# Kernel optimization log

Measured on AMD Instinct MI355X. Metric: run time of the kernel, lower is better.

## Reference

```python
import jax, jax.numpy as jnp
import numpy as np

N, E, F, H = 20000, 320000, 128, 256   # nodes, edges, in-features, hidden
M, NQ = 4096, 2048                      # lsq rows, QP variables
LAMB_MAX = 2.0


def setup_inputs() -> dict:
    key = jax.random.key(0)
    ks = jax.random.split(key, 12)
    x = jax.random.normal(ks[0], (N, F), jnp.float32)
    edge_index = jax.random.randint(ks[1], (2, E), 0, N)
    A = jax.random.normal(ks[2], (M, NQ), jnp.float32) * 0.05
    b = jax.random.normal(ks[3], (M, 1), jnp.float32)
    feat_ids = jax.random.randint(ks[4], (NQ,), 0, N)
    x_prior = jax.random.uniform(ks[5], (NQ, 1), jnp.float32)
    lamb = jnp.ones((1,), jnp.float32)
    # ChebConv K=2 weights: one linear per Chebyshev order, plus bias
    W10 = jax.random.normal(ks[6], (F, H), jnp.float32) / np.sqrt(F)
    W11 = jax.random.normal(ks[7], (F, H), jnp.float32) / np.sqrt(F)
    b1 = jnp.zeros((H,), jnp.float32)
    W20 = jax.random.normal(ks[8], (H, 1), jnp.float32) / np.sqrt(H)
    W21 = jax.random.normal(ks[9], (H, 1), jnp.float32) / np.sqrt(H)
    b2 = jnp.zeros((1,), jnp.float32)
    return {"x": x, "edge_index": edge_index, "A": A, "b": b,
            "feat_ids": feat_ids, "x_prior": x_prior, "lamb": lamb,
            "W10": W10, "W11": W11, "b1": b1,
            "W20": W20, "W21": W21, "b2": b2}


def _cheb_conv(x, edge_index, W0, W1, bias, lam_max):
    """PyG ChebConv with K=2: out = x @ W0 + (2L/lam_max - I) x @ W1 + bias,
    L = I - D^{-1/2} A D^{-1/2}, via edge gather/scatter (no dense NxN)."""
    row, col = edge_index[0], edge_index[1]
    n = x.shape[0]
    deg = jax.ops.segment_sum(jnp.ones_like(row, dtype=x.dtype), row, num_segments=n)
    dinv = jnp.where(deg > 0, deg ** -0.5, 0.0)
    # normalized edge weight scaled by 2/lam_max, negated (off-diag of L_hat)
    w = -(2.0 / lam_max) * dinv[row] * dinv[col]              # [E]
    msg = jax.ops.segment_sum(w[:, None] * x[col], row, num_segments=n)
    Tx1 = msg + (2.0 / lam_max - 1.0) * x                      # diagonal of L_hat
    return x @ W0 + Tx1 @ W1 + bias


def reference(x, edge_index, A, b, feat_ids, x_prior, lamb,
              W10, W11, b1, W20, W21, b2):
    h = jax.nn.relu(_cheb_conv(x, edge_index, W10, W11, b1, LAMB_MAX))
    h = lamb[0] * jax.nn.relu(_cheb_conv(h, edge_index, W20, W21, b2, LAMB_MAX))
    hfold = h[feat_ids] + 1e-5                                 # [NQ, 1]
    q = hfold[:, 0]
    # QP: min 1/2 z^T Q z + p^T z with vacuous inequality (0*z <= 0.1) and no
    # equality constraints -> interior-point converges to unconstrained min.
    Q = A.T @ A + jnp.diag(q)                                  # [NQ, NQ]
    p = -(x_prior * hfold)[:, 0] - (b.T @ A)[0]                # [NQ]
    z = jnp.linalg.solve(Q, -p)                                # [NQ]
    return z[:, None]                                          # f.T -> [NQ, 1]
```

## Files before the change

kernel.cpp:

```cpp
#include <hip/hip_runtime.h>

#define N_NODES 20000
#define N_EDGES 320000
#define F_DIM   128
#define H_DIM   256
#define M_ROWS  4096
#define NQ      2048
#define NIT     18
#define MM_ROWS 20032

typedef __attribute__((ext_vector_type(8))) short short8;
typedef __attribute__((ext_vector_type(4))) float f32x4;


__device__ __forceinline__ float wred(float v) {
#pragma unroll
  for (int m = 32; m > 0; m >>= 1) v += __shfl_xor(v, m, 64);
  return v;
}

__device__ __forceinline__ float bred256(float v, float* lds) {
  v = wred(v);
  int w = threadIdx.x >> 6;
  if ((threadIdx.x & 63) == 0) lds[w] = v;
  __syncthreads();
  float tot = lds[0] + lds[1] + lds[2] + lds[3];
  __syncthreads();
  return tot;
}

__device__ __forceinline__ unsigned f2bf(float f) {
  unsigned u = __float_as_uint(f);
  unsigned r = u + 0x7fffu + ((u >> 16) & 1u);
  return r >> 16;
}
__device__ __forceinline__ float bflo(unsigned u) { return __uint_as_float(u << 16); }
__device__ __forceinline__ float bfhi(unsigned u) { return __uint_as_float(u & 0xffff0000u); }


__global__ __launch_bounds__(256) void k_deg(const int* __restrict__ ei, int* __restrict__ deg) {
  int e = blockIdx.x * 256 + threadIdx.x;
  if (e < N_EDGES) atomicAdd(&deg[ei[e]], 1);
}

__global__ __launch_bounds__(1024) void k_scan(const int* __restrict__ deg,
    int* __restrict__ rowstart, float* __restrict__ dinv) {
  __shared__ int part[1024];
  int t = threadIdx.x;
  const int chunk = (N_NODES + 1023) / 1024;
  int lo = t * chunk;
  int hi = lo + chunk; if (hi > N_NODES) hi = N_NODES;
  int s = 0;
  for (int i = lo; i < hi; ++i) {
    int d = deg[i];
    dinv[i] = d > 0 ? rsqrtf((float)d) : 0.f;
    s += d;
  }
  part[t] = s;
  __syncthreads();
  for (int off = 1; off < 1024; off <<= 1) {
    int v = part[t];
    int add = (t >= off) ? part[t - off] : 0;
    __syncthreads();
    part[t] = v + add;
    __syncthreads();
  }
  int base = (t > 0) ? part[t - 1] : 0;
  for (int i = lo; i < hi; ++i) { rowstart[i] = base; base += deg[i]; }
  if (t == 0) rowstart[N_NODES] = part[1023];
}

__global__ __launch_bounds__(256) void k_scatter(const int* __restrict__ ei,
    const int* __restrict__ rowstart, int* __restrict__ cursor,
    const float* __restrict__ dinv, int* __restrict__ cols, float* __restrict__ wvals) {
  int e = blockIdx.x * 256 + threadIdx.x;
  if (e >= N_EDGES) return;
  int r = ei[e];
  int c = ei[N_EDGES + e];
  int pos = rowstart[r] + atomicAdd(&cursor[r], 1);
  cols[pos] = c;
  wvals[pos] = -dinv[r] * dinv[c];
}

#define CONVX_BLKS (MM_ROWS * 16 / 256)

__global__ __launch_bounds__(256) void k_pack(const float* __restrict__ x,
    const float* __restrict__ W10, const float* __restrict__ W11,
    unsigned* __restrict__ xu, unsigned* __restrict__ Wtb) {
  int bx = blockIdx.x;
  if (bx < CONVX_BLKS) {
    int gid = bx * 256 + threadIdx.x;
    int row = gid >> 4;
    int q8 = gid & 15;
    uint4* xu4 = (uint4*)xu;
    if (row < N_NODES) {
      const float4* x4 = (const float4*)x;
      float4 a = x4[(size_t)row * 32 + q8 * 2];
      float4 b = x4[(size_t)row * 32 + q8 * 2 + 1];
      uint4 u;
      u.x = f2bf(a.x) | (f2bf(a.y) << 16);
      u.y = f2bf(a.z) | (f2bf(a.w) << 16);
      u.z = f2bf(b.x) | (f2bf(b.y) << 16);
      u.w = f2bf(b.z) | (f2bf(b.w) << 16);
      xu4[(size_t)row * 32 + q8] = u;
    } else {
      uint4 z = make_uint4(0, 0, 0, 0);
      xu4[(size_t)row * 32 + q8] = z;
      xu4[(size_t)row * 32 + 16 + q8] = z;
    }
  } else {
    int gid = (bx - CONVX_BLKS) * 256 + threadIdx.x;
    int n = gid >> 7;
    int u = gid & 127;
    int k0 = u * 2;
    float v0 = (k0 < 128) ? W10[(size_t)k0 * H_DIM + n]
                          : W11[(size_t)(k0 - 128) * H_DIM + n];
    float v1 = (k0 + 1 < 128) ? W10[(size_t)(k0 + 1) * H_DIM + n]
                              : W11[(size_t)(k0 - 127) * H_DIM + n];
    Wtb[(size_t)n * 128 + u] = f2bf(v0) | (f2bf(v1) << 16);
  }
}

__global__ __launch_bounds__(256) void k_msg1(const int* __restrict__ rowstart,
    const int* __restrict__ cols, const float* __restrict__ wvals,
    unsigned* __restrict__ xu) {
  int wid = (blockIdx.x * 256 + threadIdx.x) >> 6;
  int lane = threadIdx.x & 63;
  if (wid >= N_NODES) return;
  int s0 = rowstart[wid], s1 = rowstart[wid + 1];
  float2 acc = make_float2(0.f, 0.f);
  for (int e = s0; e < s1; ++e) {
    int c = cols[e];
    float w = wvals[e];
    unsigned u = xu[(size_t)c * 128 + lane];
    acc.x += w * bflo(u);
    acc.y += w * bfhi(u);
  }
  xu[(size_t)wid * 128 + 64 + lane] = f2bf(acc.x) | (f2bf(acc.y) << 16);
}

#define WS_ST 20

__global__ __launch_bounds__(256) void k_mm(const unsigned* __restrict__ xu,
    const unsigned* __restrict__ Wtb, const float* __restrict__ b1,
    const float* __restrict__ W20, const float* __restrict__ W21,
    float* __restrict__ t, float* __restrict__ s) {
  __shared__ unsigned Ws[2][256 * WS_ST];
  const int row0 = blockIdx.x * 64;
  const int tid = threadIdx.x;
  const int w = tid >> 6, lane = tid & 63;
  const int colb = w * 64;
  const int frow = lane & 15, fqo = (lane >> 4) * 4;
  const int c16 = lane & 15, q4 = lane >> 4;

  f32x4 acc[4][4];
#pragma unroll
  for (int a = 0; a < 4; ++a)
#pragma unroll
    for (int b = 0; b < 4; ++b) {
      acc[a][b][0] = 0.f; acc[a][b][1] = 0.f;
      acc[a][b][2] = 0.f; acc[a][b][3] = 0.f;
    }

  const uint4* Wtb4 = (const uint4*)Wtb;
  uint4 rw[4];
#pragma unroll
  for (int j = 0; j < 4; ++j) rw[j] = Wtb4[(size_t)tid * 32 + j];

  for (int kc = 0; kc < 8; ++kc) {
    const int b = kc & 1;
    unsigned* dst = Ws[b] + tid * WS_ST;
#pragma unroll
    for (int j = 0; j < 4; ++j) *(uint4*)(dst + j * 4) = rw[j];
    if (kc + 1 < 8) {
#pragma unroll
      for (int j = 0; j < 4; ++j) rw[j] = Wtb4[(size_t)tid * 32 + (kc + 1) * 4 + j];
    }
    __syncthreads();
    short8 af[4], bf[4];
#pragma unroll
    for (int a = 0; a < 4; ++a)
      af[a] = *(const short8*)(xu + (size_t)(row0 + a * 16 + frow) * 128 + kc * 16 + fqo);
#pragma unroll
    for (int n = 0; n < 4; ++n)
      bf[n] = *(const short8*)(Ws[b] + (colb + n * 16 + frow) * WS_ST + fqo);
#pragma unroll
    for (int a = 0; a < 4; ++a)
#pragma unroll
      for (int n = 0; n < 4; ++n)
        acc[a][n] = __builtin_amdgcn_mfma_f32_16x16x32_bf16(af[a], bf[n], acc[a][n], 0, 0, 0);
    __syncthreads();
  }

  float tp[4][4] = {}, sp[4][4] = {};
#pragma unroll
  for (int b2 = 0; b2 < 4; ++b2) {
    int gc = colb + b2 * 16 + c16;
    float w20 = W20[gc], w21 = W21[gc], bb = b1[gc];
#pragma unroll
    for (int a = 0; a < 4; ++a)
#pragma unroll
      for (int r = 0; r < 4; ++r) {
        float val = acc[a][b2][r] + bb;
        val = val > 0.f ? val : 0.f;
        tp[a][r] += val * w20;
        sp[a][r] += val * w21;
      }
  }
#pragma unroll
  for (int a = 0; a < 4; ++a)
#pragma unroll
    for (int r = 0; r < 4; ++r) {
#pragma unroll
      for (int m = 1; m < 16; m <<= 1) {
        tp[a][r] += __shfl_xor(tp[a][r], m, 64);
        sp[a][r] += __shfl_xor(sp[a][r], m, 64);
      }
    }
  if (c16 == 0) {
#pragma unroll
    for (int a = 0; a < 4; ++a)
#pragma unroll
      for (int r = 0; r < 4; ++r) {
        int gr = row0 + a * 16 + q4 * 4 + r;
        if (gr < N_NODES) {
          atomicAdd(&t[gr], tp[a][r]);
          atomicAdd(&s[gr], sp[a][r]);
        }
      }
  }
}


__global__ __launch_bounds__(256) void k_h2(const float* __restrict__ t,
    const float* __restrict__ s, const int* __restrict__ rowstart,
    const int* __restrict__ cols, const float* __restrict__ wvals,
    const float* __restrict__ lamb, const float* __restrict__ b2, float* __restrict__ h2) {
  int i = blockIdx.x * 256 + threadIdx.x;
  if (i >= N_NODES) return;
  float m = 0.f;
  int s0 = rowstart[i], s1 = rowstart[i + 1];
  for (int e = s0; e < s1; ++e) m += wvals[e] * s[cols[e]];
  float val = t[i] + m + b2[0];
  val = val > 0.f ? val : 0.f;
  h2[i] = lamb[0] * val;
}

__global__ __launch_bounds__(256) void k_prep(const float* __restrict__ A,
    const float* __restrict__ b, unsigned* __restrict__ Atu, float* __restrict__ btA_parts) {
  int jp = blockIdx.x * 256 + threadIdx.x;
  int k0 = blockIdx.y * 128;
  const float2* A2 = (const float2*)A;
  float acc0 = 0.f, acc1 = 0.f;
  for (int kk = 0; kk < 128; kk += 8) {
    float ax[8], ay[8];
#pragma unroll
    for (int i = 0; i < 8; ++i) {
      int k = k0 + kk + i;
      float2 a = A2[(size_t)k * 1024 + jp];
      float bk = b[k];
      acc0 += a.x * bk;
      acc1 += a.y * bk;
      ax[i] = a.x; ay[i] = a.y;
    }
    uint4 t0, t1;
    t0.x = f2bf(ax[0]) | (f2bf(ax[1]) << 16);
    t0.y = f2bf(ax[2]) | (f2bf(ax[3]) << 16);
    t0.z = f2bf(ax[4]) | (f2bf(ax[5]) << 16);
    t0.w = f2bf(ax[6]) | (f2bf(ax[7]) << 16);
    t1.x = f2bf(ay[0]) | (f2bf(ay[1]) << 16);
    t1.y = f2bf(ay[2]) | (f2bf(ay[3]) << 16);
    t1.z = f2bf(ay[4]) | (f2bf(ay[5]) << 16);
    t1.w = f2bf(ay[6]) | (f2bf(ay[7]) << 16);
    int uoff = (k0 + kk) >> 1;
    *(uint4*)(Atu + (size_t)(2 * jp) * 2048 + uoff) = t0;
    *(uint4*)(Atu + (size_t)(2 * jp + 1) * 2048 + uoff) = t1;
  }
  ((float2*)(btA_parts + (size_t)blockIdx.y * NQ))[jp] = make_float2(acc0, acc1);
}

__global__ __launch_bounds__(256) void k_qrhs(const float* __restrict__ h2,
    const int* __restrict__ feat_ids, const float* __restrict__ x_prior,
    const float* __restrict__ btA_parts, float* __restrict__ q, float* __restrict__ r) {
  int j = blockIdx.x * 256 + threadIdx.x;
  int f = feat_ids[j];
  float hf = h2[f] + 1e-5f;
  q[j] = hf;
  float bta = 0.f;
#pragma unroll
  for (int c = 0; c < 32; ++c) bta += btA_parts[(size_t)c * NQ + j];
  r[j] = x_prior[j] * hf + bta;
}

#define GR_ST 20

__global__ __launch_bounds__(512) void k_gram(const unsigned* __restrict__ Atu,
                                              float* __restrict__ Gp) {
  __shared__ unsigned shmem[10240];
  const int i0 = blockIdx.x * 128, j0 = blockIdx.y * 128;
  const int kz = blockIdx.z;
  const int tid = threadIdx.x;
  const int grp = tid >> 8;
  const int t8 = tid & 255;
  const int w = tid >> 6;
  const int wt = w & 3;
  const int lane = tid & 63;
  const int wr = (wt >> 1) * 64, wc = (wt & 1) * 64;
  const int srow = t8 >> 1, suo = (t8 & 1) * 8;
  const int frow = lane & 15, fqo = (lane >> 4) * 4;

  unsigned* shA = shmem + grp * 5120;
  unsigned* shB = shA + 2560;

  f32x4 acc[4][4];
#pragma unroll
  for (int a = 0; a < 4; ++a)
#pragma unroll
    for (int b = 0; b < 4; ++b) {
      acc[a][b][0] = 0.f; acc[a][b][1] = 0.f;
      acc[a][b][2] = 0.f; acc[a][b][3] = 0.f;
    }

  const unsigned* pa = Atu + (size_t)(i0 + srow) * 2048 + kz * 1024 + suo;
  const unsigned* pb = Atu + (size_t)(j0 + srow) * 2048 + kz * 1024 + suo;

  int ku = grp * 16;
  uint4 ra0 = *(const uint4*)(pa + ku);
  uint4 ra1 = *(const uint4*)(pa + ku + 4);
  uint4 rb0 = *(const uint4*)(pb + ku);
  uint4 rb1 = *(const uint4*)(pb + ku + 4);

  for (int si = 0; si < 32; ++si) {
    unsigned* as = shA + srow * GR_ST + suo;
    unsigned* bs = shB + srow * GR_ST + suo;
    *(uint4*)as = ra0; *(uint4*)(as + 4) = ra1;
    *(uint4*)bs = rb0; *(uint4*)(bs + 4) = rb1;
    if (si + 1 < 32) {
      ku = (si + 1) * 32 + grp * 16;
      ra0 = *(const uint4*)(pa + ku);
      ra1 = *(const uint4*)(pa + ku + 4);
      rb0 = *(const uint4*)(pb + ku);
      rb1 = *(const uint4*)(pb + ku + 4);
    }
    __syncthreads();
    short8 af[4], bf[4];
#pragma unroll
    for (int a = 0; a < 4; ++a)
      af[a] = *(const short8*)(shA + (wr + a * 16 + frow) * GR_ST + fqo);
#pragma unroll
    for (int b2 = 0; b2 < 4; ++b2)
      bf[b2] = *(const short8*)(shB + (wc + b2 * 16 + frow) * GR_ST + fqo);
#pragma unroll
    for (int a = 0; a < 4; ++a)
#pragma unroll
      for (int b2 = 0; b2 < 4; ++b2)
        acc[a][b2] = __builtin_amdgcn_mfma_f32_16x16x32_bf16(af[a], bf[b2], acc[a][b2], 0, 0, 0);
    __syncthreads();
  }

  const int q4 = lane >> 4, c16 = lane & 15;
  float* comb = (float*)shmem;
#pragma unroll
  for (int rnd = 0; rnd < 2; ++rnd) {
    if (grp == 1 && (wt >> 1) == rnd) {
      float* dst = comb + (wt & 1) * 4160;
#pragma unroll
      for (int a = 0; a < 4; ++a)
#pragma unroll
        for (int b2 = 0; b2 < 4; ++b2)
#pragma unroll
          for (int r = 0; r < 4; ++r)
            dst[(a * 16 + q4 * 4 + r) * 65 + b2 * 16 + c16] = acc[a][b2][r];
    }
    __syncthreads();
    if (grp == 0 && (wt >> 1) == rnd) {
      const float* src = comb + (wt & 1) * 4160;
#pragma unroll
      for (int a = 0; a < 4; ++a)
#pragma unroll
        for (int b2 = 0; b2 < 4; ++b2)
#pragma unroll
          for (int r = 0; r < 4; ++r)
            acc[a][b2][r] += src[(a * 16 + q4 * 4 + r) * 65 + b2 * 16 + c16];
    }
    __syncthreads();
  }

  if (grp == 0) {
    float* Gz = Gp + (size_t)kz * NQ * NQ;
#pragma unroll
    for (int a = 0; a < 4; ++a)
#pragma unroll
      for (int b2 = 0; b2 < 4; ++b2)
#pragma unroll
        for (int r = 0; r < 4; ++r) {
          int gr = i0 + wr + a * 16 + q4 * 4 + r;
          int gc = j0 + wc + b2 * 16 + c16;
          Gz[(size_t)gr * NQ + gc] = acc[a][b2][r];
        }
  }
}

__global__ __launch_bounds__(256) void k_gconv(const float* __restrict__ G0,
    const float* __restrict__ G1, const float* __restrict__ q,
    unsigned* __restrict__ Gb, float* __restrict__ qcorr) {
  int row = blockIdx.x;
  int tid = threadIdx.x;
  const float4* g04 = (const float4*)(G0 + (size_t)row * NQ);
  const float4* g14 = (const float4*)(G1 + (size_t)row * NQ);
  float4 a0 = g04[tid * 2], b0 = g04[tid * 2 + 1];
  float4 a1 = g14[tid * 2], b1 = g14[tid * 2 + 1];
  float v[8] = {a0.x + a1.x, a0.y + a1.y, a0.z + a1.z, a0.w + a1.w,
                b0.x + b1.x, b0.y + b1.y, b0.z + b1.z, b0.w + b1.w};
  bool diag = ((row >> 3) == tid);
  if (diag) v[row & 7] += q[row];
  uint4 u;
  u.x = f2bf(v[0]) | (f2bf(v[1]) << 16);
  u.y = f2bf(v[2]) | (f2bf(v[3]) << 16);
  u.z = f2bf(v[4]) | (f2bf(v[5]) << 16);
  u.w = f2bf(v[6]) | (f2bf(v[7]) << 16);
  ((uint4*)(Gb + (size_t)row * 1024))[tid] = u;
  if (diag) {
    float vd = v[row & 7];
    qcorr[row] = vd - __uint_as_float(f2bf(vd) << 16);
  }
}

__global__ __launch_bounds__(256) void k_cgG(int k, const unsigned* __restrict__ Gb,
    const float* __restrict__ qcorr,
    const float* __restrict__ r_old, float* __restrict__ r_new,
    const float* __restrict__ p_old, float* __restrict__ p_new,
    const float* __restrict__ Qp_in, float* __restrict__ Qp_out,
    float* __restrict__ xcg) {
  __shared__ float pshare[NQ];
  __shared__ float lds[4];
  const int tid = threadIdx.x, bid = blockIdx.x;
  const float4* r4 = (const float4*)r_old;
  float4 ra = r4[tid * 2], rb2 = r4[tid * 2 + 1];
  float pv[8];
  if (k == 0) {
    pv[0] = ra.x; pv[1] = ra.y; pv[2] = ra.z; pv[3] = ra.w;
    pv[4] = rb2.x; pv[5] = rb2.y; pv[6] = rb2.z; pv[7] = rb2.w;
    if (bid == 0) {
      ((float4*)p_new)[tid * 2] = ra;
      ((float4*)p_new)[tid * 2 + 1] = rb2;
    }
  } else {
    const float4* p4 = (const float4*)p_old;
    const float4* qp4 = (const float4*)Qp_in;
    float4 pa = p4[tid * 2], pb = p4[tid * 2 + 1];
    float4 qa = qp4[tid * 2], qb = qp4[tid * 2 + 1];
    float rr = ra.x * ra.x + ra.y * ra.y + ra.z * ra.z + ra.w * ra.w +
               rb2.x * rb2.x + rb2.y * rb2.y + rb2.z * rb2.z + rb2.w * rb2.w;
    float pap = pa.x * qa.x + pa.y * qa.y + pa.z * qa.z + pa.w * qa.w +
                pb.x * qb.x + pb.y * qb.y + pb.z * qb.z + pb.w * qb.w;
    rr = bred256(rr, lds);
    pap = bred256(pap, lds);
    float alpha = rr / pap;
    if (bid == 0) {
      float4* x4 = (float4*)xcg;
      float4 xa = x4[tid * 2], xb = x4[tid * 2 + 1];
      xa.x += alpha * pa.x; xa.y += alpha * pa.y;
      xa.z += alpha * pa.z; xa.w += alpha * pa.w;
      xb.x += alpha * pb.x; xb.y += alpha * pb.y;
      xb.z += alpha * pb.z; xb.w += alpha * pb.w;
      x4[tid * 2] = xa; x4[tid * 2 + 1] = xb;
    }
    ra.x -= alpha * qa.x; ra.y -= alpha * qa.y;
    ra.z -= alpha * qa.z; ra.w -= alpha * qa.w;
    rb2.x -= alpha * qb.x; rb2.y -= alpha * qb.y;
    rb2.z -= alpha * qb.z; rb2.w -= alpha * qb.w;
    float rrn = ra.x * ra.x + ra.y * ra.y + ra.z * ra.z + ra.w * ra.w +
                rb2.x * rb2.x + rb2.y * rb2.y + rb2.z * rb2.z + rb2.w * rb2.w;
    rrn = bred256(rrn, lds);
    float beta = rrn / rr;
    pv[0] = ra.x + beta * pa.x; pv[1] = ra.y + beta * pa.y;
    pv[2] = ra.z + beta * pa.z; pv[3] = ra.w + beta * pa.w;
    pv[4] = rb2.x + beta * pb.x; pv[5] = rb2.y + beta * pb.y;
    pv[6] = rb2.z + beta * pb.z; pv[7] = rb2.w + beta * pb.w;
    if (bid == 0) {
      ((float4*)r_new)[tid * 2] = ra;
      ((float4*)r_new)[tid * 2 + 1] = rb2;
      ((float4*)p_new)[tid * 2] = make_float4(pv[0], pv[1], pv[2], pv[3]);
      ((float4*)p_new)[tid * 2 + 1] = make_float4(pv[4], pv[5], pv[6], pv[7]);
    }
  }
  ((float4*)pshare)[tid * 2] = make_float4(pv[0], pv[1], pv[2], pv[3]);
  ((float4*)pshare)[tid * 2 + 1] = make_float4(pv[4], pv[5], pv[6], pv[7]);
  __syncthreads();
  const int w = tid >> 6, lane = tid & 63;
  const int row = bid * 4 + w;
  const uint4* Gr = (const uint4*)(Gb + (size_t)row * 1024);
  const float4* ps4 = (const float4*)pshare;
  float acc = 0.f;
#pragma unroll
  for (int c = 0; c < 4; ++c) {
    uint4 gv = Gr[c * 64 + lane];
    float4 pa = ps4[c * 128 + lane * 2];
    float4 pb = ps4[c * 128 + lane * 2 + 1];
    acc += bflo(gv.x) * pa.x + bfhi(gv.x) * pa.y;
    acc += bflo(gv.y) * pa.z + bfhi(gv.y) * pa.w;
    acc += bflo(gv.z) * pb.x + bfhi(gv.z) * pb.y;
    acc += bflo(gv.w) * pb.z + bfhi(gv.w) * pb.w;
  }
  acc = wred(acc);
  if (lane == 0) Qp_out[row] = acc + qcorr[row] * pshare[row];
}

__global__ __launch_bounds__(256) void k_cgfin(const float* __restrict__ r_last,
    const float* __restrict__ p_last, const float* __restrict__ Qp,
    const float* __restrict__ xcg, float* __restrict__ out) {
  const int tid = threadIdx.x;
  const int lane = tid & 63;
  const float4* r4 = (const float4*)r_last;
  const float4* p4 = (const float4*)p_last;
  const float4* q4 = (const float4*)Qp;
  float rr = 0.f, pap = 0.f;
#pragma unroll
  for (int c = 0; c < 4; ++c) {
#pragma unroll
    for (int hh = 0; hh < 2; ++hh) {
      float4 rv = r4[c * 128 + lane * 2 + hh];
      float4 pv = p4[c * 128 + lane * 2 + hh];
      float4 qv = q4[c * 128 + lane * 2 + hh];
      rr += rv.x * rv.x + rv.y * rv.y + rv.z * rv.z + rv.w * rv.w;
      pap += pv.x * qv.x + pv.y * qv.y + pv.z * qv.z + pv.w * qv.w;
    }
  }
  rr = wred(rr);
  pap = wred(pap);
  float alpha = rr / pap;
  const float4* x4 = (const float4*)xcg;
  float4* o4 = (float4*)out;
#pragma unroll
  for (int hh = 0; hh < 2; ++hh) {
    int i4 = tid * 2 + hh;
    float4 xv = x4[i4];
    float4 pv = p4[i4];
    xv.x += alpha * pv.x; xv.y += alpha * pv.y;
    xv.z += alpha * pv.z; xv.w += alpha * pv.w;
    o4[i4] = xv;
  }
}


extern "C" void kernel_launch(void* const* d_in, const int* in_sizes, int n_in,
                              void* d_out, int out_size, void* d_ws, size_t ws_size,
                              hipStream_t stream) {
  const float* x      = (const float*)d_in[0];
  const int*   ei     = (const int*)d_in[1];
  const float* A      = (const float*)d_in[2];
  const float* b      = (const float*)d_in[3];
  const int*   fids   = (const int*)d_in[4];
  const float* xprior = (const float*)d_in[5];
  const float* lamb   = (const float*)d_in[6];
  const float* W10    = (const float*)d_in[7];
  const float* W11    = (const float*)d_in[8];
  const float* b1     = (const float*)d_in[9];
  const float* W20    = (const float*)d_in[10];
  const float* W21    = (const float*)d_in[11];
  const float* b2     = (const float*)d_in[12];
  float* out = (float*)d_out;

  char* base = (char*)d_ws;
  size_t o = 0;
  auto alloc = [&](size_t bytes) { size_t r = o; o = (o + bytes + 255) & ~size_t(255); return r; };

  size_t off_deg    = alloc(N_NODES * 4);
  size_t off_cursor = alloc(N_NODES * 4);
  size_t off_xcg    = alloc(NQ * 4);
  size_t off_t      = alloc(N_NODES * 4);
  size_t off_s      = alloc(N_NODES * 4);
  size_t zero_end   = o;
  size_t off_rowst  = alloc((N_NODES + 1) * 4);
  size_t off_dinv   = alloc(N_NODES * 4);
  size_t off_h2     = alloc(N_NODES * 4);
  size_t off_q      = alloc(NQ * 4);
  size_t off_r0     = alloc(NQ * 4);
  size_t off_r1     = alloc(NQ * 4);
  size_t off_p0     = alloc(NQ * 4);
  size_t off_p1     = alloc(NQ * 4);
  size_t off_Qp0    = alloc(NQ * 4);
  size_t off_Qp1    = alloc(NQ * 4);
  size_t off_qcorr  = alloc(NQ * 4);
  size_t off_btAp   = alloc(32 * NQ * 4);
  size_t off_Wtb    = alloc(256 * 128 * 4);
  size_t sz_cols  = (size_t)N_EDGES * 4 + 256;
  size_t sz_wvals = (size_t)N_EDGES * 4 + 256;
  size_t sz_xmsg  = (size_t)MM_ROWS * 256 * 2;
  size_t union_gnn = sz_cols + sz_wvals + sz_xmsg;
  size_t union_at  = (size_t)M_ROWS * NQ * 2;
  size_t off_union = alloc(union_gnn > union_at ? union_gnn : union_at);
  size_t off_G0    = alloc((size_t)NQ * NQ * 4);
  size_t off_G1    = alloc((size_t)NQ * NQ * 4);
  if (o > ws_size) return;

  int*   deg      = (int*)(base + off_deg);
  int*   cursor   = (int*)(base + off_cursor);
  float* xcg      = (float*)(base + off_xcg);
  float* t        = (float*)(base + off_t);
  float* s        = (float*)(base + off_s);
  int*   rowstart = (int*)(base + off_rowst);
  float* dinv     = (float*)(base + off_dinv);
  float* h2       = (float*)(base + off_h2);
  float* q        = (float*)(base + off_q);
  float* rb[2]    = {(float*)(base + off_r0), (float*)(base + off_r1)};
  float* pg[2]    = {(float*)(base + off_p0), (float*)(base + off_p1)};
  float* Qpb[2]   = {(float*)(base + off_Qp0), (float*)(base + off_Qp1)};
  float* qcorr    = (float*)(base + off_qcorr);
  float* btA_parts = (float*)(base + off_btAp);
  unsigned* Wtb   = (unsigned*)(base + off_Wtb);
  int*   cols     = (int*)(base + off_union);
  float* wvals    = (float*)(base + off_union + sz_cols);
  unsigned* xmsgb = (unsigned*)(base + off_union + sz_cols + sz_wvals);
  unsigned* Atu   = (unsigned*)(base + off_union);
  unsigned* Gb    = (unsigned*)(base + off_union);
  float* G0       = (float*)(base + off_G0);
  float* G1       = (float*)(base + off_G1);

  hipMemsetAsync(d_ws, 0, zero_end, stream);

  k_deg<<<(N_EDGES + 255) / 256, 256, 0, stream>>>(ei, deg);
  k_scan<<<1, 1024, 0, stream>>>(deg, rowstart, dinv);
  k_scatter<<<(N_EDGES + 255) / 256, 256, 0, stream>>>(ei, rowstart, cursor, dinv, cols, wvals);

  k_pack<<<CONVX_BLKS + 128, 256, 0, stream>>>(x, W10, W11, xmsgb, Wtb);
  k_msg1<<<N_NODES / 4, 256, 0, stream>>>(rowstart, cols, wvals, xmsgb);
  k_mm<<<MM_ROWS / 64, 256, 0, stream>>>(xmsgb, Wtb, b1, W20, W21, t, s);
  k_h2<<<(N_NODES + 255) / 256, 256, 0, stream>>>(t, s, rowstart, cols, wvals, lamb, b2, h2);

  k_prep<<<dim3(4, 32), 256, 0, stream>>>(A, b, Atu, btA_parts);
  k_qrhs<<<NQ / 256, 256, 0, stream>>>(h2, fids, xprior, btA_parts, q, rb[0]);
  k_gram<<<dim3(16, 16, 2), 512, 0, stream>>>(Atu, G0);
  k_gconv<<<NQ, 256, 0, stream>>>(G0, G1, q, Gb, qcorr);

  k_cgG<<<512, 256, 0, stream>>>(0, Gb, qcorr, rb[0], rb[0], pg[0], pg[0],
                                 Qpb[1], Qpb[0], xcg);
  for (int k = 1; k < NIT; ++k) {
    k_cgG<<<512, 256, 0, stream>>>(k, Gb, qcorr, rb[(k - 1) & 1], rb[k & 1],
                                   pg[(k - 1) & 1], pg[k & 1],
                                   Qpb[(k - 1) & 1], Qpb[k & 1], xcg);
  }
  k_cgfin<<<1, 256, 0, stream>>>(rb[(NIT - 1) & 1], pg[(NIT - 1) & 1],
                                 Qpb[(NIT - 1) & 1], xcg, out);
}
```

Before: 412.3 us.

## Exploit Gram symmetry: compute upper-triangle tiles with 4-way K split, mirror in conversion

The Gram kernel now computes only the 136 upper-triangular 128x128 tiles of A^T A, with the K dimension split four ways instead of two. Partial tiles are stored compactly. The conversion kernel sums the four partials, adds the diagonal q, writes bf16, and writes the transposed off-diagonal tile through an LDS transpose. This roughly halves the matmul work and the fp32 partial traffic, at the cost of an extra partial buffer and uncoalesced-ish transposed stores.

```diff
diff --git a/kernel.cpp b/kernel.cpp
--- a/kernel.cpp
+++ b/kernel.cpp
@@ -293,12 +293,16 @@
 }
 
 #define GR_ST 20
+#define NTILE 136
 
 __global__ __launch_bounds__(512) void k_gram(const unsigned* __restrict__ Atu,
                                               float* __restrict__ Gp) {
   __shared__ unsigned shmem[10240];
-  const int i0 = blockIdx.x * 128, j0 = blockIdx.y * 128;
-  const int kz = blockIdx.z;
+  int uu = blockIdx.x, bi = 0;
+  while (uu >= 16 - bi) { uu -= 16 - bi; ++bi; }
+  const int bj = bi + uu;
+  const int i0 = bi * 128, j0 = bj * 128;
+  const int kq = blockIdx.y;
   const int tid = threadIdx.x;
   const int grp = tid >> 8;
   const int t8 = tid & 255;
@@ -321,8 +325,8 @@
       acc[a][b][2] = 0.f; acc[a][b][3] = 0.f;
     }
 
-  const unsigned* pa = Atu + (size_t)(i0 + srow) * 2048 + kz * 1024 + suo;
-  const unsigned* pb = Atu + (size_t)(j0 + srow) * 2048 + kz * 1024 + suo;
+  const unsigned* pa = Atu + (size_t)(i0 + srow) * 2048 + kq * 512 + suo;
+  const unsigned* pb = Atu + (size_t)(j0 + srow) * 2048 + kq * 512 + suo;
 
   int ku = grp * 16;
   uint4 ra0 = *(const uint4*)(pa + ku);
@@ -330,12 +334,12 @@
   uint4 rb0 = *(const uint4*)(pb + ku);
   uint4 rb1 = *(const uint4*)(pb + ku + 4);
 
-  for (int si = 0; si < 32; ++si) {
+  for (int si = 0; si < 16; ++si) {
     unsigned* as = shA + srow * GR_ST + suo;
     unsigned* bs = shB + srow * GR_ST + suo;
     *(uint4*)as = ra0; *(uint4*)(as + 4) = ra1;
     *(uint4*)bs = rb0; *(uint4*)(bs + 4) = rb1;
-    if (si + 1 < 32) {
+    if (si + 1 < 16) {
       ku = (si + 1) * 32 + grp * 16;
       ra0 = *(const uint4*)(pa + ku);
       ra1 = *(const uint4*)(pa + ku + 4);
@@ -387,42 +391,77 @@
   }
 
   if (grp == 0) {
-    float* Gz = Gp + (size_t)kz * NQ * NQ;
+    float* Gz = Gp + ((size_t)kq * NTILE + blockIdx.x) * 16384;
 #pragma unroll
     for (int a = 0; a < 4; ++a)
 #pragma unroll
       for (int b2 = 0; b2 < 4; ++b2)
 #pragma unroll
         for (int r = 0; r < 4; ++r) {
-          int gr = i0 + wr + a * 16 + q4 * 4 + r;
-          int gc = j0 + wc + b2 * 16 + c16;
-          Gz[(size_t)gr * NQ + gc] = acc[a][b2][r];
+          int lr = wr + a * 16 + q4 * 4 + r;
+          int lc = wc + b2 * 16 + c16;
+          Gz[lr * 128 + lc] = acc[a][b2][r];
         }
   }
 }
 
-__global__ __launch_bounds__(256) void k_gconv(const float* __restrict__ G0,
-    const float* __restrict__ G1, const float* __restrict__ q,
-    unsigned* __restrict__ Gb, float* __restrict__ qcorr) {
-  int row = blockIdx.x;
-  int tid = threadIdx.x;
-  const float4* g04 = (const float4*)(G0 + (size_t)row * NQ);
-  const float4* g14 = (const float4*)(G1 + (size_t)row * NQ);
-  float4 a0 = g04[tid * 2], b0 = g04[tid * 2 + 1];
-  float4 a1 = g14[tid * 2], b1 = g14[tid * 2 + 1];
-  float v[8] = {a0.x + a1.x, a0.y + a1.y, a0.z + a1.z, a0.w + a1.w,
-                b0.x + b1.x, b0.y + b1.y, b0.z + b1.z, b0.w + b1.w};
-  bool diag = ((row >> 3) == tid);
-  if (diag) v[row & 7] += q[row];
-  uint4 u;
-  u.x = f2bf(v[0]) | (f2bf(v[1]) << 16);
-  u.y = f2bf(v[2]) | (f2bf(v[3]) << 16);
-  u.z = f2bf(v[4]) | (f2bf(v[5]) << 16);
-  u.w = f2bf(v[6]) | (f2bf(v[7]) << 16);
-  ((uint4*)(Gb + (size_t)row * 1024))[tid] = u;
-  if (diag) {
-    float vd = v[row & 7];
-    qcorr[row] = vd - __uint_as_float(f2bf(vd) << 16);
+#define GT_ST 131
+
+__global__ __launch_bounds__(256) void k_gconv(const float* __restrict__ Gp,
+    const float* __restrict__ q, unsigned* __restrict__ Gb, float* __restrict__ qcorr) {
+  __shared__ unsigned short T[128 * GT_ST];
+  int uu = blockIdx.x, bi = 0;
+  while (uu >= 16 - bi) { uu -= 16 - bi; ++bi; }
+  const int bj = bi + uu;
+  const int tid = threadIdx.x;
+  const int r = tid >> 1, ch = (tid & 1) * 64;
+  const size_t tile = (size_t)blockIdx.x * 16384;
+  const float4* P0 = (const float4*)(Gp + tile + r * 128 + ch);
+  const float4* P1 = (const float4*)(Gp + (size_t)1 * NTILE * 16384 + tile + r * 128 + ch);
+  const float4* P2 = (const float4*)(Gp + (size_t)2 * NTILE * 16384 + tile + r * 128 + ch);
+  const float4* P3 = (const float4*)(Gp + (size_t)3 * NTILE * 16384 + tile + r * 128 + ch);
+  const int gr = bi * 128 + r;
+  const bool hasdiag = (bi == bj) && (r >= ch) && (r < ch + 64);
+  unsigned uo[32];
+#pragma unroll
+  for (int j = 0; j < 16; ++j) {
+    float4 a = P0[j], b = P1[j], c = P2[j], d = P3[j];
+    float v0 = a.x + b.x + c.x + d.x;
+    float v1 = a.y + b.y + c.y + d.y;
+    float v2 = a.z + b.z + c.z + d.z;
+    float v3 = a.w + b.w + c.w + d.w;
+    const int c0 = ch + j * 4;
+    if (hasdiag && (r - c0 >= 0) && (r - c0 < 4)) {
+      float qv = q[gr];
+      int dsel = r - c0;
+      if (dsel == 0) v0 += qv;
+      else if (dsel == 1) v1 += qv;
+      else if (dsel == 2) v2 += qv;
+      else v3 += qv;
+      float vd = (dsel == 0) ? v0 : (dsel == 1) ? v1 : (dsel == 2) ? v2 : v3;
+      qcorr[gr] = vd - bflo(f2bf(vd));
+    }
+    unsigned u0 = f2bf(v0) | (f2bf(v1) << 16);
+    unsigned u1 = f2bf(v2) | (f2bf(v3) << 16);
+    uo[2 * j] = u0;
+    uo[2 * j + 1] = u1;
+    T[r * GT_ST + c0]     = (unsigned short)(u0 & 0xffffu);
+    T[r * GT_ST + c0 + 1] = (unsigned short)(u0 >> 16);
+    T[r * GT_ST + c0 + 2] = (unsigned short)(u1 & 0xffffu);
+    T[r * GT_ST + c0 + 3] = (unsigned short)(u1 >> 16);
+  }
+  uint4* dst = (uint4*)(Gb + (size_t)gr * 1024 + bj * 64 + (ch >> 1));
+#pragma unroll
+  for (int j = 0; j < 8; ++j) dst[j] = ((const uint4*)uo)[j];
+  __syncthreads();
+  if (bi != bj) {
+    const int wv = tid >> 6, lane = tid & 63;
+    for (int kk = 0; kk < 32; ++kk) {
+      int rr = kk * 4 + wv;
+      unsigned lo = T[(2 * lane) * GT_ST + rr];
+      unsigned hi = T[(2 * lane + 1) * GT_ST + rr];
+      Gb[(size_t)(bj * 128 + rr) * 1024 + bi * 64 + lane] = lo | (hi << 16);
+    }
   }
 }
 
@@ -591,8 +630,7 @@
   size_t union_gnn = sz_cols + sz_wvals + sz_xmsg;
   size_t union_at  = (size_t)M_ROWS * NQ * 2;
   size_t off_union = alloc(union_gnn > union_at ? union_gnn : union_at);
-  size_t off_G0    = alloc((size_t)NQ * NQ * 4);
-  size_t off_G1    = alloc((size_t)NQ * NQ * 4);
+  size_t off_Gp    = alloc((size_t)4 * NTILE * 16384 * 4);
   if (o > ws_size) return;
 
   int*   deg      = (int*)(base + off_deg);
@@ -615,8 +653,7 @@
   unsigned* xmsgb = (unsigned*)(base + off_union + sz_cols + sz_wvals);
   unsigned* Atu   = (unsigned*)(base + off_union);
   unsigned* Gb    = (unsigned*)(base + off_union);
-  float* G0       = (float*)(base + off_G0);
-  float* G1       = (float*)(base + off_G1);
+  float* Gp       = (float*)(base + off_Gp);
 
   hipMemsetAsync(d_ws, 0, zero_end, stream);
 
@@ -631,8 +668,8 @@
 
   k_prep<<<dim3(4, 32), 256, 0, stream>>>(A, b, Atu, btA_parts);
   k_qrhs<<<NQ / 256, 256, 0, stream>>>(h2, fids, xprior, btA_parts, q, rb[0]);
-  k_gram<<<dim3(16, 16, 2), 512, 0, stream>>>(Atu, G0);
-  k_gconv<<<NQ, 256, 0, stream>>>(G0, G1, q, Gb, qcorr);
+  k_gram<<<dim3(NTILE, 4), 512, 0, stream>>>(Atu, Gp);
+  k_gconv<<<NTILE, 256, 0, stream>>>(Gp, q, Gb, qcorr);
 
   k_cgG<<<512, 256, 0, stream>>>(0, Gb, qcorr, rb[0], rb[0], pg[0], pg[0],
                                  Qpb[1], Qpb[0], xcg);
```

Result: no change. 415.1 us (+0.7%).
